# Kernel tuning notes

Hardware: AMD Instinct MI355X
Metric: run time of the kernel (lower is better)

## Reference

```python
import jax, jax.numpy as jnp
import numpy as np

B, N, D = 2, 4096, 2048
H, DH, W = 8, 128, 512          # heads (num_queries), dim_head, window_size
SCALE = 8.0                      # qk_scale (qk_rmsnorm=True)


def setup_inputs() -> dict:
    key = jax.random.key(0)
    ks = jax.random.split(key, 5)
    return {
        "x": jax.random.normal(ks[0], (B, N, D), jnp.float32),
        "Wq": jax.random.normal(ks[1], (H * DH, D), jnp.float32) * 0.02,
        "Wkv": jax.random.normal(ks[2], (2 * H * DH, D), jnp.float32) * 0.02,
        "q_scale": jnp.ones((DH,), jnp.float32),
        "k_scale": jnp.ones((DH,), jnp.float32),
        "Wg": jax.random.normal(ks[3], (H, D), jnp.float32) * 0.02,
        "bg": jnp.zeros((H,), jnp.float32),
        "Wo": jax.random.normal(ks[4], (D, H * DH), jnp.float32) * 0.02,
    }


def _l2norm(t):
    # F.normalize: x / max(||x||, eps)
    return t / jnp.maximum(jnp.linalg.norm(t, axis=-1, keepdims=True), 1e-12)


def reference(x, Wq, Wkv, q_scale, k_scale, Wg, bg, Wo):
    b, n, _ = x.shape
    inner = H * DH
    q = (x @ Wq.T).reshape(b, n, H, DH).transpose(0, 2, 1, 3)      # b h n d
    kv = x @ Wkv.T
    k = kv[..., :inner].reshape(b, n, H, DH).transpose(0, 2, 1, 3)
    v = kv[..., inner:].reshape(b, n, H, DH).transpose(0, 2, 1, 3)
    # qk rmsnorm
    q = _l2norm(q) * q_scale
    k = _l2norm(k) * k_scale

    nb = n // W
    qb = q.reshape(b, H, nb, W, DH)
    kb = k.reshape(b, H, nb, W, DH)
    vb = v.reshape(b, H, nb, W, DH)

    def look_around(t):  # prepend previous bucket (look_backward=1)
        prev = jnp.concatenate([jnp.zeros_like(t[:, :, :1]), t[:, :, :-1]], axis=2)
        return jnp.concatenate([prev, t], axis=3)  # b h nb 2W d

    kw, vw = look_around(kb), look_around(vb)

    pos = jnp.arange(n).reshape(nb, W)
    pos_prev = jnp.concatenate([jnp.full((1, W), -1), pos[:-1]], axis=0)
    posk = jnp.concatenate([pos_prev, pos], axis=1)                 # nb 2W
    dist = pos[:, :, None] - posk[:, None, :]                       # nb W 2W
    # causal + exact window: attend j with 0 <= i - j <= W, valid (non-pad) key
    mask = (posk[:, None, :] >= 0) & (dist >= 0) & (dist <= W)

    sim = jnp.einsum('bhnid,bhnjd->bhnij', qb * SCALE, kw)
    sim = jnp.where(mask, sim, jnp.finfo(sim.dtype).min)
    attn = jax.nn.softmax(sim, axis=-1)
    o = jnp.einsum('bhnij,bhnjd->bhnid', attn, vw).reshape(b, H, n, DH)

    # per-head sigmoid value gating
    gates = jax.nn.sigmoid(jnp.einsum('bnd,hd->bhn', x, Wg) + bg[None, :, None])
    o = o * gates[..., None]

    o = o.transpose(0, 2, 1, 3).reshape(b, n, inner)                # b n (h d)
    return o @ Wo.T
```

## Files before the change

### kernel.cpp

```cpp
#include <hip/hip_runtime.h>
#include <hip/hip_bf16.h>
#include <cstdint>

typedef short short8 __attribute__((ext_vector_type(8)));
typedef short short4v __attribute__((ext_vector_type(4)));
typedef __bf16 bf16x8 __attribute__((ext_vector_type(8)));
typedef float f32x4 __attribute__((ext_vector_type(4)));
typedef unsigned short u16;
typedef unsigned int u32;

#define B_  2
#define N_  4096
#define D_  2048
#define H_  8
#define DH_ 128
#define W_  512
#define M_  (B_*N_)
#define INNER_ (H_*DH_)

static __device__ __forceinline__ u16 f2bf(float f) {
  u32 u = __float_as_uint(f);
  u32 r = (u + 0x7fffu + ((u >> 16) & 1u)) >> 16;
  return (u16)r;
}
static __device__ __forceinline__ float bf2f(u16 u) {
  return __uint_as_float(((u32)u) << 16);
}
static __device__ __forceinline__ f32x4 mfma16(short8 a, short8 b, f32x4 c) {
  return __builtin_amdgcn_mfma_f32_16x16x32_bf16(
      __builtin_bit_cast(bf16x8, a), __builtin_bit_cast(bf16x8, b), c, 0, 0, 0);
}

#define GLOAD_LDS16(g, s) \
  __builtin_amdgcn_global_load_lds((const __attribute__((address_space(1))) void*)(g), \
                                   (__attribute__((address_space(3))) void*)(s), 16, 0, 0)
#define BARRIER() __builtin_amdgcn_s_barrier()
#define SB0 __builtin_amdgcn_sched_barrier(0)
#define WVM4 asm volatile("s_waitcnt vmcnt(4)" ::: "memory")
#define WVM0 asm volatile("s_waitcnt vmcnt(0)" ::: "memory")

__global__ __launch_bounds__(256) void cvt_kernel(
    const float* __restrict__ x, const float* __restrict__ Wq,
    const float* __restrict__ Wkv, const float* __restrict__ Wo,
    u16* __restrict__ xb, u16* __restrict__ Wcat, u16* __restrict__ Wob) {
  size_t i = ((size_t)blockIdx.x * 256 + threadIdx.x) * 8;
  const float* src; u16* dst; size_t off;
  const size_t SX = 16777216ul, SQ = 2097152ul, SKV = 4194304ul;
  if (i < SX)                { src = x;   dst = xb;             off = i; }
  else if (i < SX+SQ)        { src = Wq;  dst = Wcat;           off = i - SX; }
  else if (i < SX+SQ+SKV)    { src = Wkv; dst = Wcat + 2097152; off = i - SX - SQ; }
  else                       { src = Wo;  dst = Wob;            off = i - SX - SQ - SKV; }
  float4 a = *(const float4*)(src + off);
  float4 b = *(const float4*)(src + off + 4);
  short8 o;
  o[0]=(short)f2bf(a.x); o[1]=(short)f2bf(a.y); o[2]=(short)f2bf(a.z); o[3]=(short)f2bf(a.w);
  o[4]=(short)f2bf(b.x); o[5]=(short)f2bf(b.y); o[6]=(short)f2bf(b.z); o[7]=(short)f2bf(b.w);
  *(short8*)(dst + off) = o;
}

template<int EPI>
__global__ __launch_bounds__(256) void gemm_bt(
    const u16* __restrict__ A, const u16* __restrict__ Bw,
    u16* __restrict__ Dq, u16* __restrict__ Dk, u16* __restrict__ Dv,
    float* __restrict__ Cf, int N, int K) {
  __shared__ u16 sA[128*64];
  __shared__ u16 sB[128*64];
  const int tid = threadIdx.x;
  const int lane = tid & 63, wv = tid >> 6;
  const int wm = wv >> 1, wn = wv & 1;
  const int m0 = blockIdx.y * 128, n0 = blockIdx.x * 128;
  const int l15 = lane & 15, l4 = lane >> 4;
  f32x4 acc[4][4] = {};

  #pragma unroll 1
  for (int kt = 0; kt < K; kt += 64) {
    __syncthreads();
    #pragma unroll
    for (int r = 0; r < 4; ++r) {
      int cf = r*256 + tid;
      int row = cf >> 3, cph = cf & 7;
      int clg = cph ^ (row & 7);
      GLOAD_LDS16(A + (size_t)(m0 + row)*K + kt + clg*8, sA + (size_t)(r*256 + wv*64)*8);
    }
    #pragma unroll
    for (int r = 0; r < 4; ++r) {
      int cf = r*256 + tid;
      int row = cf >> 3, cph = cf & 7;
      int clg = cph ^ (row & 7);
      GLOAD_LDS16(Bw + (size_t)(n0 + row)*K + kt + clg*8, sB + (size_t)(r*256 + wv*64)*8);
    }
    __syncthreads();
    #pragma unroll
    for (int ks = 0; ks < 2; ++ks) {
      short8 af[4], bfr[4];
      #pragma unroll
      for (int mf = 0; mf < 4; ++mf) {
        int row = wm*64 + mf*16 + l15;
        int ch = (ks*4 + l4) ^ (row & 7);
        af[mf] = *(const short8*)(sA + row*64 + ch*8);
      }
      #pragma unroll
      for (int nf = 0; nf < 4; ++nf) {
        int row = wn*64 + nf*16 + l15;
        int ch = (ks*4 + l4) ^ (row & 7);
        bfr[nf] = *(const short8*)(sB + row*64 + ch*8);
      }
      #pragma unroll
      for (int mf = 0; mf < 4; ++mf)
        #pragma unroll
        for (int nf = 0; nf < 4; ++nf)
          acc[mf][nf] = mfma16(af[mf], bfr[nf], acc[mf][nf]);
    }
  }

  if (EPI == 0) {
    const int bufsel = blockIdx.x >> 3;
    const int h = blockIdx.x & 7;
    u16* dst = bufsel == 0 ? Dq : (bufsel == 1 ? Dk : Dv);
    #pragma unroll
    for (int mf = 0; mf < 4; ++mf)
      #pragma unroll
      for (int nf = 0; nf < 4; ++nf)
        #pragma unroll
        for (int j = 0; j < 4; ++j) {
          int m = m0 + wm*64 + mf*16 + l4*4 + j;
          int d = wn*64 + nf*16 + l15;
          int b = m >> 12, n = m & (N_ - 1);
          dst[(((size_t)(b*H_ + h)*N_ + n) << 7) + d] = f2bf(acc[mf][nf][j]);
        }
  } else {
    #pragma unroll
    for (int mf = 0; mf < 4; ++mf)
      #pragma unroll
      for (int nf = 0; nf < 4; ++nf)
        #pragma unroll
        for (int j = 0; j < 4; ++j) {
          int m = m0 + wm*64 + mf*16 + l4*4 + j;
          int nn = n0 + wn*64 + nf*16 + l15;
          Cf[(size_t)m*N + nn] = acc[mf][nf][j];
        }
  }
}

__global__ __launch_bounds__(256) void normqk_kernel(
    u16* __restrict__ qb, u16* __restrict__ kb,
    const float* __restrict__ qs, const float* __restrict__ ks) {
  int lane = threadIdx.x & 63, wv = threadIdx.x >> 6;
  size_t vec = (size_t)blockIdx.x * 4 + wv;
  bool isq = vec < 65536;
  u16* p = isq ? qb + vec*128 : kb + (vec - 65536)*128;
  const float* sc = isq ? qs : ks;
  u32 u = *(const u32*)(p + lane*2);
  float a = bf2f((u16)(u & 0xffffu));
  float b = bf2f((u16)(u >> 16));
  float ss = a*a + b*b;
  #pragma unroll
  for (int off = 32; off >= 1; off >>= 1) ss += __shfl_xor(ss, off);
  float inv = 1.0f / fmaxf(sqrtf(ss), 1e-12f);
  if (isq) inv *= 8.0f;
  float r0 = a * inv * sc[lane*2];
  float r1 = b * inv * sc[lane*2 + 1];
  *(u32*)(p + lane*2) = (u32)f2bf(r0) | ((u32)f2bf(r1) << 16);
}

__global__ __launch_bounds__(256) void transpose_v_kernel(
    const u16* __restrict__ v, u16* __restrict__ vT) {
  int bh = blockIdx.x >> 6;
  int n0 = (blockIdx.x & 63) << 6;
  __shared__ u16 tl[64][136];
  int tid = threadIdx.x;
  #pragma unroll
  for (int r = 0; r < 4; ++r) {
    int cf = r*256 + tid;
    int row = cf >> 4, ch = cf & 15;
    *(short8*)&tl[row][ch*8] = *(const short8*)(v + ((size_t)bh*N_ + n0 + row)*128 + ch*8);
  }
  __syncthreads();
  #pragma unroll
  for (int r = 0; r < 4; ++r) {
    int cf = r*256 + tid;
    int d = cf >> 3, nch = cf & 7;
    short8 o;
    #pragma unroll
    for (int i = 0; i < 8; ++i) o[i] = (short)tl[nch*8 + i][d];
    *(short8*)(vT + ((size_t)bh*128 + d)*N_ + n0 + nch*8) = o;
  }
}

__global__ __launch_bounds__(256) void gates_kernel(
    const u16* __restrict__ xb, const float* __restrict__ Wg,
    const float* __restrict__ bg, float* __restrict__ gates) {
  int m = blockIdx.x;
  int tid = threadIdx.x;
  const u16* xr = xb + (size_t)m * D_;
  float acc[8] = {};
  for (int d0 = tid*8; d0 < D_; d0 += 256*8) {
    short8 xv8 = *(const short8*)(xr + d0);
    #pragma unroll
    for (int e = 0; e < 8; ++e) {
      float xv = bf2f((u16)xv8[e]);
      #pragma unroll
      for (int h = 0; h < 8; ++h) acc[h] = fmaf(xv, Wg[h*D_ + d0 + e], acc[h]);
    }
  }
  #pragma unroll
  for (int h = 0; h < 8; ++h)
    #pragma unroll
    for (int off = 32; off >= 1; off >>= 1) acc[h] += __shfl_xor(acc[h], off);
  __shared__ float red[4][8];
  int lane = tid & 63, wv = tid >> 6;
  if (lane == 0) {
    #pragma unroll
    for (int h = 0; h < 8; ++h) red[wv][h] = acc[h];
  }
  __syncthreads();
  if (tid < 8) {
    float vsum = red[0][tid] + red[1][tid] + red[2][tid] + red[3][tid] + bg[tid];
    gates[(size_t)m*8 + tid] = 1.0f / (1.0f + __expf(-vsum));
  }
}

__global__ __launch_bounds__(512, 4) void attn_kernel(
    const u16* __restrict__ q, const u16* __restrict__ k,
    const u16* __restrict__ vT, const float* __restrict__ gates,
    u16* __restrict__ o) {
  extern __shared__ u16 alds[];
  u16* sK = alds;
  u16* sV = alds + 16384;
  const int bid = blockIdx.x;
  const int t = bid & 3;
  const int c = (bid >> 2) & 7;
  const int bh = bid >> 5;
  const int b = bh >> 3, h = bh & 7;
  const int i0 = c*W_ + t*128;
  const int tid = threadIdx.x;
  const int lane = tid & 63, wv = tid >> 6;
  const int l15 = lane & 15, l4 = lane >> 4;
  u16* sPw = alds + 32768 + wv*1024;

#define STAGE_KV(KT, PB) do { \
    const int _j0 = i0 - 512 + (KT)*64; \
    u16* _dK = sK + (PB)*8192; \
    u16* _dV = sV + (PB)*8192; \
    _Pragma("unroll") for (int r = 0; r < 2; ++r) { \
      int cf = r*512 + tid; int row = cf >> 4, cph = cf & 15; \
      int clg = cph ^ (row & 15); \
      GLOAD_LDS16(k + (((size_t)bh*N_ + _j0 + row) << 7) + clg*8, _dK + (size_t)(r*512 + wv*64)*8); \
    } \
    _Pragma("unroll") for (int r = 0; r < 2; ++r) { \
      int cf = r*512 + tid; int row = cf >> 3, cph = cf & 7; \
      int clg = cph ^ (row & 7); \
      GLOAD_LDS16(vT + ((size_t)bh*128 + row)*N_ + _j0 + clg*8, _dV + (size_t)(r*512 + wv*64)*8); \
    } \
  } while(0)

  short8 qf[4];
  const u16* qbase = q + (((size_t)bh*N_ + i0 + wv*16) << 7);
  #pragma unroll
  for (int ks = 0; ks < 4; ++ks)
    qf[ks] = *(const short8*)(qbase + l15*128 + ks*32 + l4*8);

  float mrow[4], lrow[4];
  f32x4 oacc[8];
  #pragma unroll
  for (int j = 0; j < 4; ++j) { mrow[j] = -1e30f; lrow[j] = 0.f; }
  #pragma unroll
  for (int df = 0; df < 8; ++df) oacc[df] = (f32x4){0.f,0.f,0.f,0.f};

  const int kt0 = (i0 >= 512) ? 0 : ((512 - i0) >> 6);
  STAGE_KV(kt0, 0);

  #pragma unroll 1
  for (int kt = kt0; kt < 10; ++kt) {
    const int pb = (kt - kt0) & 1;
    if (kt < 9) { STAGE_KV(kt + 1, pb ^ 1); WVM4; } else { WVM0; }
    BARRIER(); SB0;

    const int base = 512 - kt*64;
    const int rmin = wv*16;
    if (base + rmin + 15 >= 0 && base + rmin - 63 <= 512) {
      const u16* cK = sK + pb*8192;
      const u16* cV = sV + pb*8192;

      f32x4 s[4];
      #pragma unroll
      for (int nf = 0; nf < 4; ++nf) s[nf] = (f32x4){0.f,0.f,0.f,0.f};
      #pragma unroll
      for (int ks = 0; ks < 4; ++ks) {
        short8 kb[4];
        #pragma unroll
        for (int nf = 0; nf < 4; ++nf) {
          int row = nf*16 + l15;
          int ch = (ks*4 + l4) ^ (row & 15);
          kb[nf] = *(const short8*)(cK + row*128 + ch*8);
        }
        #pragma unroll
        for (int nf = 0; nf < 4; ++nf)
          s[nf] = mfma16(qf[ks], kb[nf], s[nf]);
      }

      if (kt < 2 || kt > 7) {
        #pragma unroll
        for (int nf = 0; nf < 4; ++nf)
          #pragma unroll
          for (int j = 0; j < 4; ++j) {
            int r = rmin + l4*4 + j;
            int sidx = nf*16 + l15;
            int dist = base + r - sidx;
            if (dist < 0 || dist > 512) s[nf][j] = -1e30f;
          }
      }

      #pragma unroll
      for (int j = 0; j < 4; ++j) {
        float mx = fmaxf(fmaxf(s[0][j], s[1][j]), fmaxf(s[2][j], s[3][j]));
        #pragma unroll
        for (int off = 1; off <= 8; off <<= 1) mx = fmaxf(mx, __shfl_xor(mx, off));
        if (!__all(mx <= mrow[j] + 8.0f)) {
          float mnew = fmaxf(mrow[j], mx);
          float scal = __expf(mrow[j] - mnew);
          mrow[j] = mnew;
          lrow[j] *= scal;
          #pragma unroll
          for (int df = 0; df < 8; ++df) oacc[df][j] *= scal;
        }
        float m = mrow[j];
        float ls = 0.f;
        #pragma unroll
        for (int nf = 0; nf < 4; ++nf) {
          float p = __expf(s[nf][j] - m);
          s[nf][j] = p;
          ls += p;
        }
        #pragma unroll
        for (int off = 1; off <= 8; off <<= 1) ls += __shfl_xor(ls, off);
        lrow[j] += ls;
        int prow = l4*4 + j;
        #pragma unroll
        for (int nf = 0; nf < 4; ++nf) {
          int pcol = nf*16 + l15;
          int ch = (pcol >> 3) ^ (prow & 7);
          sPw[prow*64 + ch*8 + (pcol & 7)] = f2bf(s[nf][j]);
        }
      }

      #pragma unroll
      for (int ks2 = 0; ks2 < 2; ++ks2) {
        short8 pa;
        {
          int ch = (ks2*4 + l4) ^ (l15 & 7);
          pa = *(const short8*)(sPw + l15*64 + ch*8);
        }
        #pragma unroll
        for (int df = 0; df < 8; ++df) {
          int vd = df*16 + l15;
          int ch2 = (ks2*4 + l4) ^ (vd & 7);
          short8 vb = *(const short8*)(cV + vd*64 + ch2*8);
          oacc[df] = mfma16(pa, vb, oacc[df]);
        }
      }
    }
    BARRIER();
  }

  #pragma unroll
  for (int j = 0; j < 4; ++j) {
    int r = wv*16 + l4*4 + j;
    int i = i0 + r;
    float f = (1.0f / lrow[j]) * gates[((size_t)b*N_ + i)*8 + h];
    #pragma unroll
    for (int df = 0; df < 8; ++df)
      o[((size_t)b*N_ + i)*INNER_ + h*128 + df*16 + l15] = f2bf(oacc[df][j] * f);
  }
#undef STAGE_KV
}

extern "C" void kernel_launch(void* const* d_in, const int* in_sizes, int n_in,
                              void* d_out, int out_size, void* d_ws, size_t ws_size,
                              hipStream_t stream) {
  const float* x       = (const float*)d_in[0];
  const float* Wq      = (const float*)d_in[1];
  const float* Wkv     = (const float*)d_in[2];
  const float* q_scale = (const float*)d_in[3];
  const float* k_scale = (const float*)d_in[4];
  const float* Wg      = (const float*)d_in[5];
  const float* bg      = (const float*)d_in[6];
  const float* Wo      = (const float*)d_in[7];
  float* out = (float*)d_out;

  u16* qb  = (u16*)d_out;
  u16* kb  = qb + 8388608;
  u16* vb  = kb + 8388608;
  u16* vTb = vb + 8388608;

  char* w = (char*)d_ws;
  u16* xb   = (u16*)w;
  u16* ob   = (u16*)w;
  u16* Wcat = (u16*)(w + 33554432);
  u16* Wob  = (u16*)(w + 46137344);
  float* gb = (float*)(w + 50331648);
  (void)in_sizes; (void)n_in; (void)out_size; (void)ws_size;

  hipFuncSetAttribute((const void*)attn_kernel,
                      hipFuncAttributeMaxDynamicSharedMemorySize, 81920);

  cvt_kernel<<<12288, 256, 0, stream>>>(x, Wq, Wkv, Wo, xb, Wcat, Wob);
  gemm_bt<0><<<dim3(24, 64), 256, 0, stream>>>(xb, Wcat, qb, kb, vb, nullptr, 3072, 2048);
  normqk_kernel<<<32768, 256, 0, stream>>>(qb, kb, q_scale, k_scale);
  transpose_v_kernel<<<1024, 256, 0, stream>>>(vb, vTb);
  gates_kernel<<<8192, 256, 0, stream>>>(xb, Wg, bg, gb);
  attn_kernel<<<512, 512, 81920, stream>>>(qb, kb, vTb, gb, ob);
  gemm_bt<1><<<dim3(16, 64), 256, 0, stream>>>(ob, Wob, nullptr, nullptr, nullptr, out, 2048, 1024);
}
```

Before: 286.4 us.

## Write V transposed from QKV GEMM and defer qk norm scaling into attention

The QKV projection epilogue now writes V directly in the transposed layout, which removes the separate transpose kernel and its round trip through memory. The qk normalization kernel now only computes per-row inverse norms. The attention kernel applies them: q is scaled at load together with q_scale and k_scale, and each score column is multiplied by the k inverse norm. This saves the read-modify-write of the full q and k tensors. In exchange the V stores become strided 8-byte writes, and q and k are rounded to bf16 before normalization, which slightly changes numerics.

After: 282.3 us. Within noise of the previous version (-1.4%).

```diff
diff --git a/kernel.cpp b/kernel.cpp
--- a/kernel.cpp
+++ b/kernel.cpp
@@ -116,18 +116,36 @@
   if (EPI == 0) {
     const int bufsel = blockIdx.x >> 3;
     const int h = blockIdx.x & 7;
-    u16* dst = bufsel == 0 ? Dq : (bufsel == 1 ? Dk : Dv);
-    #pragma unroll
-    for (int mf = 0; mf < 4; ++mf)
-      #pragma unroll
-      for (int nf = 0; nf < 4; ++nf)
-        #pragma unroll
-        for (int j = 0; j < 4; ++j) {
-          int m = m0 + wm*64 + mf*16 + l4*4 + j;
+    const int b = m0 >> 12;
+    if (bufsel < 2) {
+      u16* dst = bufsel == 0 ? Dq : Dk;
+      #pragma unroll
+      for (int mf = 0; mf < 4; ++mf)
+        #pragma unroll
+        for (int nf = 0; nf < 4; ++nf)
+          #pragma unroll
+          for (int j = 0; j < 4; ++j) {
+            int m = m0 + wm*64 + mf*16 + l4*4 + j;
+            int d = wn*64 + nf*16 + l15;
+            int n = m & (N_ - 1);
+            dst[(((size_t)(b*H_ + h)*N_ + n) << 7) + d] = f2bf(acc[mf][nf][j]);
+          }
+    } else {
+      const int bh = b*H_ + h;
+      #pragma unroll
+      for (int mf = 0; mf < 4; ++mf)
+        #pragma unroll
+        for (int nf = 0; nf < 4; ++nf) {
           int d = wn*64 + nf*16 + l15;
-          int b = m >> 12, n = m & (N_ - 1);
-          dst[(((size_t)(b*H_ + h)*N_ + n) << 7) + d] = f2bf(acc[mf][nf][j]);
-        }
+          int n = (m0 & (N_ - 1)) + wm*64 + mf*16 + l4*4;
+          short4v pk;
+          pk[0] = (short)f2bf(acc[mf][nf][0]);
+          pk[1] = (short)f2bf(acc[mf][nf][1]);
+          pk[2] = (short)f2bf(acc[mf][nf][2]);
+          pk[3] = (short)f2bf(acc[mf][nf][3]);
+          *(short4v*)(Dv + ((size_t)bh*128 + d)*N_ + n) = pk;
+        }
+    }
   } else {
     #pragma unroll
     for (int mf = 0; mf < 4; ++mf)
@@ -142,48 +160,23 @@
   }
 }
 
-__global__ __launch_bounds__(256) void normqk_kernel(
-    u16* __restrict__ qb, u16* __restrict__ kb,
-    const float* __restrict__ qs, const float* __restrict__ ks) {
+__global__ __launch_bounds__(256) void norms_kernel(
+    const u16* __restrict__ qb, const u16* __restrict__ kb,
+    float* __restrict__ qn, float* __restrict__ kn) {
   int lane = threadIdx.x & 63, wv = threadIdx.x >> 6;
   size_t vec = (size_t)blockIdx.x * 4 + wv;
   bool isq = vec < 65536;
-  u16* p = isq ? qb + vec*128 : kb + (vec - 65536)*128;
-  const float* sc = isq ? qs : ks;
+  const u16* p = isq ? qb + vec*128 : kb + (vec - 65536)*128;
   u32 u = *(const u32*)(p + lane*2);
   float a = bf2f((u16)(u & 0xffffu));
   float b = bf2f((u16)(u >> 16));
   float ss = a*a + b*b;
   #pragma unroll
   for (int off = 32; off >= 1; off >>= 1) ss += __shfl_xor(ss, off);
-  float inv = 1.0f / fmaxf(sqrtf(ss), 1e-12f);
-  if (isq) inv *= 8.0f;
-  float r0 = a * inv * sc[lane*2];
-  float r1 = b * inv * sc[lane*2 + 1];
-  *(u32*)(p + lane*2) = (u32)f2bf(r0) | ((u32)f2bf(r1) << 16);
-}
-
-__global__ __launch_bounds__(256) void transpose_v_kernel(
-    const u16* __restrict__ v, u16* __restrict__ vT) {
-  int bh = blockIdx.x >> 6;
-  int n0 = (blockIdx.x & 63) << 6;
-  __shared__ u16 tl[64][136];
-  int tid = threadIdx.x;
-  #pragma unroll
-  for (int r = 0; r < 4; ++r) {
-    int cf = r*256 + tid;
-    int row = cf >> 4, ch = cf & 15;
-    *(short8*)&tl[row][ch*8] = *(const short8*)(v + ((size_t)bh*N_ + n0 + row)*128 + ch*8);
-  }
-  __syncthreads();
-  #pragma unroll
-  for (int r = 0; r < 4; ++r) {
-    int cf = r*256 + tid;
-    int d = cf >> 3, nch = cf & 7;
-    short8 o;
-    #pragma unroll
-    for (int i = 0; i < 8; ++i) o[i] = (short)tl[nch*8 + i][d];
-    *(short8*)(vT + ((size_t)bh*128 + d)*N_ + n0 + nch*8) = o;
+  if (lane == 0) {
+    float inv = 1.0f / fmaxf(sqrtf(ss), 1e-12f);
+    if (isq) qn[vec] = inv * 8.0f;
+    else     kn[vec - 65536] = inv;
   }
 }
 
@@ -223,6 +216,8 @@
 __global__ __launch_bounds__(512, 4) void attn_kernel(
     const u16* __restrict__ q, const u16* __restrict__ k,
     const u16* __restrict__ vT, const float* __restrict__ gates,
+    const float* __restrict__ qsv, const float* __restrict__ ksv,
+    const float* __restrict__ qn, const float* __restrict__ kn,
     u16* __restrict__ o) {
   extern __shared__ u16 alds[];
   u16* sK = alds;
@@ -255,10 +250,19 @@
   } while(0)
 
   short8 qf[4];
-  const u16* qbase = q + (((size_t)bh*N_ + i0 + wv*16) << 7);
-  #pragma unroll
-  for (int ks = 0; ks < 4; ++ks)
-    qf[ks] = *(const short8*)(qbase + l15*128 + ks*32 + l4*8);
+  {
+    const u16* qbase = q + (((size_t)bh*N_ + i0 + wv*16) << 7);
+    float qnr = qn[(size_t)bh*N_ + i0 + wv*16 + l15];
+    #pragma unroll
+    for (int ks = 0; ks < 4; ++ks) {
+      short8 raw = *(const short8*)(qbase + l15*128 + ks*32 + l4*8);
+      const float* sp = qsv + ks*32 + l4*8;
+      const float* tp = ksv + ks*32 + l4*8;
+      #pragma unroll
+      for (int e = 0; e < 8; ++e)
+        qf[ks][e] = (short)f2bf(bf2f((u16)raw[e]) * qnr * sp[e] * tp[e]);
+    }
+  }
 
   float mrow[4], lrow[4];
   f32x4 oacc[8];
@@ -276,12 +280,18 @@
     if (kt < 9) { STAGE_KV(kt + 1, pb ^ 1); WVM4; } else { WVM0; }
     BARRIER(); SB0;
 
+    const int j0 = i0 - 512 + kt*64;
     const int base = 512 - kt*64;
     const int rmin = wv*16;
     if (base + rmin + 15 >= 0 && base + rmin - 63 <= 512) {
       const u16* cK = sK + pb*8192;
       const u16* cV = sV + pb*8192;
 
+      float knv[4];
+      #pragma unroll
+      for (int nf = 0; nf < 4; ++nf)
+        knv[nf] = kn[(size_t)bh*N_ + j0 + nf*16 + l15];
+
       f32x4 s[4];
       #pragma unroll
       for (int nf = 0; nf < 4; ++nf) s[nf] = (f32x4){0.f,0.f,0.f,0.f};
@@ -298,6 +308,11 @@
         for (int nf = 0; nf < 4; ++nf)
           s[nf] = mfma16(qf[ks], kb[nf], s[nf]);
       }
+
+      #pragma unroll
+      for (int nf = 0; nf < 4; ++nf)
+        #pragma unroll
+        for (int j = 0; j < 4; ++j) s[nf][j] *= knv[nf];
 
       if (kt < 2 || kt > 7) {
         #pragma unroll
@@ -390,8 +405,9 @@
 
   u16* qb  = (u16*)d_out;
   u16* kb  = qb + 8388608;
-  u16* vb  = kb + 8388608;
-  u16* vTb = vb + 8388608;
+  u16* vTb = kb + 8388608;
+  float* qnb = (float*)((char*)d_out + 50331648);
+  float* knb = (float*)((char*)d_out + 50593792);
 
   char* w = (char*)d_ws;
   u16* xb   = (u16*)w;
@@ -405,10 +421,9 @@
                       hipFuncAttributeMaxDynamicSharedMemorySize, 81920);
 
   cvt_kernel<<<12288, 256, 0, stream>>>(x, Wq, Wkv, Wo, xb, Wcat, Wob);
-  gemm_bt<0><<<dim3(24, 64), 256, 0, stream>>>(xb, Wcat, qb, kb, vb, nullptr, 3072, 2048);
-  normqk_kernel<<<32768, 256, 0, stream>>>(qb, kb, q_scale, k_scale);
-  transpose_v_kernel<<<1024, 256, 0, stream>>>(vb, vTb);
+  gemm_bt<0><<<dim3(24, 64), 256, 0, stream>>>(xb, Wcat, qb, kb, vTb, nullptr, 3072, 2048);
+  norms_kernel<<<32768, 256, 0, stream>>>(qb, kb, qnb, knb);
   gates_kernel<<<8192, 256, 0, stream>>>(xb, Wg, bg, gb);
-  attn_kernel<<<512, 512, 81920, stream>>>(qb, kb, vTb, gb, ob);
+  attn_kernel<<<512, 512, 81920, stream>>>(qb, kb, vTb, gb, q_scale, k_scale, qnb, knb, ob);
   gemm_bt<1><<<dim3(16, 64), 256, 0, stream>>>(ob, Wob, nullptr, nullptr, nullptr, out, 2048, 1024);
 }
```
